# Kernel optimization log

Hardware: AMD Instinct MI355X
Metric: run time of the kernel (lower is better)

The kernel has to match this reference:

```python
import jax, jax.numpy as jnp
import numpy as np

ALPHA = 0.2        # LeakyReLU negative slope
MASK_VAL = -9e15   # matches torch zero_vec constant
B, N, F, H, D = 32, 1024, 64, 3, 16  # batch, nodes, in_features, heads, head_dim


def setup_inputs() -> dict:
    key = jax.random.key(0)
    k1, k2, k3 = jax.random.split(key, 3)
    h = jax.random.normal(k1, (B, N, F), dtype=jnp.float32)
    adj = jnp.ones((N, N), dtype=jnp.float32)  # fully-connected graph ('full')
    W = jax.random.normal(k2, (H, F, D), dtype=jnp.float32) * 0.15  # ~xavier gain 1.414
    a = jax.random.normal(k3, (H, 2 * D, 1), dtype=jnp.float32) * 0.25
    return {"h": h, "adj": adj, "W": W, "a": a}


def reference(h, adj, W, a):
    # Multi-head GAT, vectorized over heads (original loops over heads).
    d = W.shape[-1]
    Wh = jnp.einsum('bnf,hfd->bhnd', h, W)              # (B,H,N,D)
    a1 = a[:, :d, 0]                                    # (H,D) -> applies to source node i
    a2 = a[:, d:, 0]                                    # (H,D) -> applies to target node j
    s1 = jnp.einsum('bhnd,hd->bhn', Wh, a1)             # (B,H,N)
    s2 = jnp.einsum('bhnd,hd->bhn', Wh, a2)             # (B,H,N)
    # e[b,h,i,j] = LeakyReLU(a1.Wh_i + a2.Wh_j) -- equivalent to the repeat/concat trick
    e = jax.nn.leaky_relu(s1[..., :, None] + s2[..., None, :], ALPHA)  # (B,H,N,N)
    e = jnp.where(adj > 0, e, MASK_VAL)
    attn = jax.nn.softmax(e, axis=-1)                   # softmax over neighbors j
    out = jnp.einsum('bhij,bhjd->bhid', attn, Wh)       # (B,H,N,D)
    # concat heads along feature dim: (B,N,H*D)
    Bn, Nn = h.shape[0], h.shape[1]
    return out.transpose(0, 2, 1, 3).reshape(Bn, Nn, -1)
```

## Files before the change

### kernel.cpp

```cpp
#include <hip/hip_runtime.h>
#include <math.h>

constexpr int Bc = 32, Nn = 1024, Fc = 64, Hc = 3, Dc = 16;
constexpr float ALPHAc = 0.2f;
constexpr float L2E    = 1.44269504088896340736f;

__device__ __forceinline__ unsigned enc_f32(float x) {
    unsigned b = __builtin_bit_cast(unsigned, x);
    return (b & 0x80000000u) ? ~b : (b | 0x80000000u);
}
__device__ __forceinline__ float dec_f32(unsigned e) {
    unsigned b = (e & 0x80000000u) ? (e ^ 0x80000000u) : ~e;
    return __builtin_bit_cast(float, b);
}

template <int CTRL, int RMASK, bool BC>
__device__ __forceinline__ float dpp_acc(float x) {
    int s = __builtin_amdgcn_update_dpp(0, __builtin_bit_cast(int, x),
                                        CTRL, RMASK, 0xF, BC);
    return x + __builtin_bit_cast(float, s);
}
__device__ __forceinline__ float wave_incl_scan(float x) {
    x = dpp_acc<0x111, 0xF, true >(x);
    x = dpp_acc<0x112, 0xF, true >(x);
    x = dpp_acc<0x114, 0xF, true >(x);
    x = dpp_acc<0x118, 0xF, true >(x);
    x = dpp_acc<0x142, 0xa, false>(x);
    x = dpp_acc<0x143, 0xc, false>(x);
    return x;
}

__global__ __launch_bounds__(1024, 8) void gat_one(
    const float* __restrict__ hbuf, const float* __restrict__ W,
    const float* __restrict__ a, const float* __restrict__ adj,
    unsigned* __restrict__ rowful, float* __restrict__ out)
{
    __shared__ __align__(16) float    PS[1025 * 11];
    __shared__ __align__(16) unsigned skA[Nn], skB[Nn];
    __shared__ __align__(16) float    s2o[Nn];
    __shared__ __align__(16) float    whs[Nn][5];
    __shared__ float    wtot[16][10];
    __shared__ unsigned wmiss[16];

    int gid = blockIdx.x;
    int bh  = gid >> 2, q = gid & 3;
    int hh  = bh % Hc,  b = bh / Hc;
    int t   = threadIdx.x;
    int wv  = t >> 6, lane = t & 63;

    int row0 = gid * 3;
    unsigned miss = 0;
#pragma unroll
    for (int rr = 0; rr < 3; ++rr) {
        int row = row0 + rr;
        if (row < Nn) {
            float av = adj[(size_t)row * Nn + t];
            miss |= (av > 0.f) ? 0u : (1u << rr);
        }
    }
#pragma unroll
    for (int off = 1; off < 64; off <<= 1)
        miss |= (unsigned)__shfl_xor((int)miss, off, 64);
    if (lane == 0) wmiss[wv] = miss;
    __syncthreads();
    if (t < 3) {
        int row = row0 + t;
        if (row < Nn) {
            unsigned m = 0;
#pragma unroll
            for (int w2 = 0; w2 < 16; ++w2) m |= wmiss[w2];
            unsigned full = ((m >> t) & 1u) ^ 1u;
            unsigned val  = 0x5AFE0000u | ((unsigned)row << 1) | full;
            __hip_atomic_store(&rowful[row], val, __ATOMIC_RELAXED,
                               __HIP_MEMORY_SCOPE_AGENT);
        }
    }

    const float4* h4 = (const float4*)(hbuf + ((size_t)b * Nn + t) * Fc);
    const float*  Wp = W + (size_t)hh * Fc * Dc;

    float acc[Dc];
#pragma unroll
    for (int d = 0; d < Dc; ++d) acc[d] = 0.f;

#pragma unroll
    for (int qq = 0; qq < Fc / 4; ++qq) {
        float4 hv = h4[qq];
#pragma unroll
        for (int c = 0; c < 4; ++c) {
            float hv1 = (c == 0) ? hv.x : (c == 1) ? hv.y : (c == 2) ? hv.z : hv.w;
            const float4* wrp = (const float4*)(Wp + (4 * qq + c) * Dc);
#pragma unroll
            for (int u = 0; u < 4; ++u) {
                float4 wq = wrp[u];
                acc[4*u+0] = fmaf(hv1, wq.x, acc[4*u+0]);
                acc[4*u+1] = fmaf(hv1, wq.y, acc[4*u+1]);
                acc[4*u+2] = fmaf(hv1, wq.z, acc[4*u+2]);
                acc[4*u+3] = fmaf(hv1, wq.w, acc[4*u+3]);
            }
        }
    }

#pragma unroll
    for (int c = 0; c < 4; ++c)
        whs[t][c] = acc[q * 4 + c];

    const float* ap = a + (size_t)hh * 2 * Dc;
    float s1v = 0.f, s2v = 0.f;
#pragma unroll
    for (int d = 0; d < Dc; ++d) {
        s1v = fmaf(acc[d], ap[d],      s1v);
        s2v = fmaf(acc[d], ap[Dc + d], s2v);
    }
    s2o[t] = s2v;

    unsigned key = (enc_f32(s2v) & ~1023u) | (unsigned)t;

#pragma unroll
    for (int k = 2; k <= 64; k <<= 1) {
#pragma unroll
        for (int s = k >> 1; s >= 1; s >>= 1) {
            unsigned other = (unsigned)__shfl_xor((int)key, s, 64);
            bool dirUp = ((t & k) == 0);
            bool lower = ((lane & s) == 0);
            unsigned mn = key < other ? key : other;
            unsigned mx = key < other ? other : key;
            key = (lower == dirUp) ? mn : mx;
        }
    }
    unsigned* bufs[2] = {skA, skB};
    int pb = 0;
#pragma unroll
    for (int k = 128; k <= 1024; k <<= 1) {
#pragma unroll
        for (int s = k >> 1; s >= 64; s >>= 1) {
            bufs[pb][t] = key;
            __syncthreads();
            unsigned other = bufs[pb][t ^ s];
            bool dirUp = ((t & k) == 0);
            bool lower = ((t & s) == 0);
            unsigned mn = key < other ? key : other;
            unsigned mx = key < other ? other : key;
            key = (lower == dirUp) ? mn : mx;
            pb ^= 1;
        }
#pragma unroll
        for (int s = 32; s >= 1; s >>= 1) {
            unsigned other = (unsigned)__shfl_xor((int)key, s, 64);
            bool dirUp = ((t & k) == 0);
            bool lower = ((lane & s) == 0);
            unsigned mn = key < other ? key : other;
            unsigned mx = key < other ? other : key;
            key = (lower == dirUp) ? mn : mx;
        }
    }
    unsigned* sorted = bufs[pb];
    sorted[t] = key;

    int   j  = key & 1023u;
    float sv = dec_f32((key & ~1023u) | 512u);
    float Bv = __builtin_amdgcn_exp2f(sv * L2E);
    float Dv = __builtin_amdgcn_exp2f(sv * (ALPHAc * L2E));
    float w0 = whs[j][0], w1 = whs[j][1], w2 = whs[j][2], w3 = whs[j][3];

    float v[10] = {Bv * w0, Bv * w1, Bv * w2, Bv * w3,
                   Dv * w0, Dv * w1, Dv * w2, Dv * w3, Bv, Dv};

#pragma unroll
    for (int c = 0; c < 10; ++c) {
        float inc = wave_incl_scan(v[c]);
        if (lane == 63) wtot[wv][c] = inc;
        v[c] = inc - v[c];
    }
    __syncthreads();

    if (t < 160) {
        int c = t >> 4, w = t & 15;
        float own = wtot[w][c];
        float x = own;
#pragma unroll
        for (int off = 1; off < 16; off <<= 1) {
            float o = __shfl_up(x, off, 16);
            if ((lane & 15) >= off) x += o;
        }
        wtot[w][c] = x - own;
        if (w == 15) PS[(size_t)1024 * 11 + c] = x;
    }
    __syncthreads();

    float* myrow = PS + (size_t)t * 11;
#pragma unroll
    for (int c = 0; c < 10; ++c)
        myrow[c] = v[c] + wtot[wv][c];
    __syncthreads();

    int i = t;
    float R  = __builtin_amdgcn_exp2f(-0.8f * L2E * s1v);
    float* op = out + ((size_t)b * Nn + i) * (Hc * Dc) + hh * Dc + q * 4;

    unsigned expv = 0x5AFE0000u | ((unsigned)i << 1) | 1u;
    unsigned fv;
    do {
        fv = __hip_atomic_load(&rowful[i], __ATOMIC_RELAXED,
                               __HIP_MEMORY_SCOPE_AGENT);
    } while ((fv | 1u) != expv);

    if (fv & 1u) {
        unsigned qk = (enc_f32(-s1v) & ~1023u) | 1023u;
        int p = 0;
#pragma unroll
        for (int step = 512; step >= 1; step >>= 1)
            if (sorted[p + step - 1] <= qk) p += step;

        const float* Pp = PS + (size_t)p * 11;
        const float* Tp = PS + (size_t)1024 * 11;
        float den = (Tp[8] - Pp[8]) + R * Pp[9];
        float inv = 1.0f / den;
        float o0 = ((Tp[0] - Pp[0]) + R * Pp[4]) * inv;
        float o1 = ((Tp[1] - Pp[1]) + R * Pp[5]) * inv;
        float o2 = ((Tp[2] - Pp[2]) + R * Pp[6]) * inv;
        float o3 = ((Tp[3] - Pp[3]) + R * Pp[7]) * inv;
        *(float4*)op = make_float4(o0, o1, o2, o3);
    } else {
        float num[4] = {0.f, 0.f, 0.f, 0.f};
        float den = 0.f;
        for (int jj = 0; jj < Nn; ++jj) {
            float aq = adj[(size_t)i * Nn + jj];
            if (aq > 0.f) {
                float sq = s2o[jj];
                float Bq = __builtin_amdgcn_exp2f(sq * L2E);
                float Dq = __builtin_amdgcn_exp2f(sq * (ALPHAc * L2E));
                float w_ = fmaxf(Bq, R * Dq);
                den += w_;
#pragma unroll
                for (int c = 0; c < 4; ++c)
                    num[c] = fmaf(w_, whs[jj][c], num[c]);
            }
        }
        float inv = 1.0f / den;
        *(float4*)op = make_float4(num[0]*inv, num[1]*inv, num[2]*inv, num[3]*inv);
    }
}

extern "C" void kernel_launch(void* const* d_in, const int* in_sizes, int n_in,
                              void* d_out, int out_size, void* d_ws, size_t ws_size,
                              hipStream_t stream)
{
    const float* hbuf = (const float*)d_in[0];
    const float* adj  = (const float*)d_in[1];
    const float* W    = (const float*)d_in[2];
    const float* a    = (const float*)d_in[3];
    float* out = (float*)d_out;

    unsigned* rowful = (unsigned*)d_ws;

    gat_one<<<dim3(Bc * Hc * 4), dim3(1024), 0, stream>>>(
        hbuf, W, a, adj, rowful, out);
}
```

Measured before the change: 41.40 us.

## Remap block indexing, prefetch h chunks, use DPP lane swaps and float4 shared Wh

Block-to-(batch, head, quarter) mapping is permuted so consecutive blocks span different batches, and only the first 256 blocks check adjacency rows, four rows each. The input feature loads are software-prefetched chunk by chunk, the smallest bitonic sort shuffles use DPP quad permutes instead of ds_bpermute, and the shared Wh slice becomes a float4 array for vector LDS access. These aim to cut shuffle latency, LDS bank traffic and load stalls. The skipped per-block barrier in non-checking blocks and the changed block order could affect how the rowful spin-wait resolves.

```diff
diff --git a/kernel.cpp b/kernel.cpp
--- a/kernel.cpp
+++ b/kernel.cpp
@@ -30,6 +30,14 @@
     return x;
 }
 
+__device__ __forceinline__ unsigned lane_xor(unsigned x, int s) {
+    if (s == 1)
+        return (unsigned)__builtin_amdgcn_update_dpp(0, (int)x, 0xB1, 0xF, 0xF, true);
+    if (s == 2)
+        return (unsigned)__builtin_amdgcn_update_dpp(0, (int)x, 0x4E, 0xF, 0xF, true);
+    return (unsigned)__shfl_xor((int)x, s, 64);
+}
+
 __global__ __launch_bounds__(1024, 8) void gat_one(
     const float* __restrict__ hbuf, const float* __restrict__ W,
     const float* __restrict__ a, const float* __restrict__ adj,
@@ -38,38 +46,38 @@
     __shared__ __align__(16) float    PS[1025 * 11];
     __shared__ __align__(16) unsigned skA[Nn], skB[Nn];
     __shared__ __align__(16) float    s2o[Nn];
-    __shared__ __align__(16) float    whs[Nn][5];
+    __shared__ __align__(16) float4   whs4[Nn];
     __shared__ float    wtot[16][10];
     __shared__ unsigned wmiss[16];
 
-    int gid = blockIdx.x;
-    int bh  = gid >> 2, q = gid & 3;
-    int hh  = bh % Hc,  b = bh / Hc;
-    int t   = threadIdx.x;
-    int wv  = t >> 6, lane = t & 63;
-
-    int row0 = gid * 3;
-    unsigned miss = 0;
-#pragma unroll
-    for (int rr = 0; rr < 3; ++rr) {
-        int row = row0 + rr;
-        if (row < Nn) {
-            float av = adj[(size_t)row * Nn + t];
+    int p  = blockIdx.x;
+    int xq = p & 7, m = p >> 3;
+    int b  = xq + 8 * (m / 12);
+    int hq = m % 12;
+    int hh = hq >> 2, q = hq & 3;
+    int bh = b * Hc + hh;
+    int t  = threadIdx.x;
+    int wv = t >> 6, lane = t & 63;
+    (void)bh;
+
+    if (p < 256) {
+        unsigned miss = 0;
+#pragma unroll
+        for (int rr = 0; rr < 4; ++rr) {
+            float av = adj[(size_t)(p * 4 + rr) * Nn + t];
             miss |= (av > 0.f) ? 0u : (1u << rr);
         }
-    }
-#pragma unroll
-    for (int off = 1; off < 64; off <<= 1)
-        miss |= (unsigned)__shfl_xor((int)miss, off, 64);
-    if (lane == 0) wmiss[wv] = miss;
-    __syncthreads();
-    if (t < 3) {
-        int row = row0 + t;
-        if (row < Nn) {
-            unsigned m = 0;
-#pragma unroll
-            for (int w2 = 0; w2 < 16; ++w2) m |= wmiss[w2];
-            unsigned full = ((m >> t) & 1u) ^ 1u;
+#pragma unroll
+        for (int off = 1; off < 64; off <<= 1)
+            miss |= (unsigned)__shfl_xor((int)miss, off, 64);
+        if (lane == 0) wmiss[wv] = miss;
+        __syncthreads();
+        if (t < 4) {
+            unsigned mm = 0;
+#pragma unroll
+            for (int w2 = 0; w2 < 16; ++w2) mm |= wmiss[w2];
+            int row = p * 4 + t;
+            unsigned full = ((mm >> t) & 1u) ^ 1u;
             unsigned val  = 0x5AFE0000u | ((unsigned)row << 1) | full;
             __hip_atomic_store(&rowful[row], val, __ATOMIC_RELAXED,
                                __HIP_MEMORY_SCOPE_AGENT);
@@ -83,27 +91,43 @@
 #pragma unroll
     for (int d = 0; d < Dc; ++d) acc[d] = 0.f;
 
-#pragma unroll
-    for (int qq = 0; qq < Fc / 4; ++qq) {
-        float4 hv = h4[qq];
-#pragma unroll
-        for (int c = 0; c < 4; ++c) {
-            float hv1 = (c == 0) ? hv.x : (c == 1) ? hv.y : (c == 2) ? hv.z : hv.w;
-            const float4* wrp = (const float4*)(Wp + (4 * qq + c) * Dc);
-#pragma unroll
-            for (int u = 0; u < 4; ++u) {
-                float4 wq = wrp[u];
-                acc[4*u+0] = fmaf(hv1, wq.x, acc[4*u+0]);
-                acc[4*u+1] = fmaf(hv1, wq.y, acc[4*u+1]);
-                acc[4*u+2] = fmaf(hv1, wq.z, acc[4*u+2]);
-                acc[4*u+3] = fmaf(hv1, wq.w, acc[4*u+3]);
+    float4 cA[4];
+#pragma unroll
+    for (int u = 0; u < 4; ++u) cA[u] = h4[u];
+
+#pragma unroll
+    for (int ch = 0; ch < 4; ++ch) {
+        float4 cB[4];
+        if (ch < 3) {
+#pragma unroll
+            for (int u = 0; u < 4; ++u) cB[u] = h4[4 * (ch + 1) + u];
+        }
+#pragma unroll
+        for (int u = 0; u < 4; ++u) {
+            float4 hv = cA[u];
+#pragma unroll
+            for (int c = 0; c < 4; ++c) {
+                float hv1 = (c == 0) ? hv.x : (c == 1) ? hv.y
+                          : (c == 2) ? hv.z : hv.w;
+                int f = ch * 16 + u * 4 + c;
+                const float4* wrp = (const float4*)(Wp + f * Dc);
+#pragma unroll
+                for (int w = 0; w < 4; ++w) {
+                    float4 wq = wrp[w];
+                    acc[4*w+0] = fmaf(hv1, wq.x, acc[4*w+0]);
+                    acc[4*w+1] = fmaf(hv1, wq.y, acc[4*w+1]);
+                    acc[4*w+2] = fmaf(hv1, wq.z, acc[4*w+2]);
+                    acc[4*w+3] = fmaf(hv1, wq.w, acc[4*w+3]);
+                }
             }
         }
-    }
-
-#pragma unroll
-    for (int c = 0; c < 4; ++c)
-        whs[t][c] = acc[q * 4 + c];
+        if (ch < 3) {
+#pragma unroll
+            for (int u = 0; u < 4; ++u) cA[u] = cB[u];
+        }
+    }
+
+    whs4[t] = make_float4(acc[q*4+0], acc[q*4+1], acc[q*4+2], acc[q*4+3]);
 
     const float* ap = a + (size_t)hh * 2 * Dc;
     float s1v = 0.f, s2v = 0.f;
@@ -120,7 +144,7 @@
     for (int k = 2; k <= 64; k <<= 1) {
 #pragma unroll
         for (int s = k >> 1; s >= 1; s >>= 1) {
-            unsigned other = (unsigned)__shfl_xor((int)key, s, 64);
+            unsigned other = lane_xor(key, s);
             bool dirUp = ((t & k) == 0);
             bool lower = ((lane & s) == 0);
             unsigned mn = key < other ? key : other;
@@ -146,7 +170,7 @@
         }
 #pragma unroll
         for (int s = 32; s >= 1; s >>= 1) {
-            unsigned other = (unsigned)__shfl_xor((int)key, s, 64);
+            unsigned other = lane_xor(key, s);
             bool dirUp = ((t & k) == 0);
             bool lower = ((lane & s) == 0);
             unsigned mn = key < other ? key : other;
@@ -161,10 +185,10 @@
     float sv = dec_f32((key & ~1023u) | 512u);
     float Bv = __builtin_amdgcn_exp2f(sv * L2E);
     float Dv = __builtin_amdgcn_exp2f(sv * (ALPHAc * L2E));
-    float w0 = whs[j][0], w1 = whs[j][1], w2 = whs[j][2], w3 = whs[j][3];
-
-    float v[10] = {Bv * w0, Bv * w1, Bv * w2, Bv * w3,
-                   Dv * w0, Dv * w1, Dv * w2, Dv * w3, Bv, Dv};
+    float4 wsl = whs4[j];
+
+    float v[10] = {Bv * wsl.x, Bv * wsl.y, Bv * wsl.z, Bv * wsl.w,
+                   Dv * wsl.x, Dv * wsl.y, Dv * wsl.z, Dv * wsl.w, Bv, Dv};
 
 #pragma unroll
     for (int c = 0; c < 10; ++c) {
@@ -207,12 +231,12 @@
 
     if (fv & 1u) {
         unsigned qk = (enc_f32(-s1v) & ~1023u) | 1023u;
-        int p = 0;
+        int pp = 0;
 #pragma unroll
         for (int step = 512; step >= 1; step >>= 1)
-            if (sorted[p + step - 1] <= qk) p += step;
-
-        const float* Pp = PS + (size_t)p * 11;
+            if (sorted[pp + step - 1] <= qk) pp += step;
+
+        const float* Pp = PS + (size_t)pp * 11;
         const float* Tp = PS + (size_t)1024 * 11;
         float den = (Tp[8] - Pp[8]) + R * Pp[9];
         float inv = 1.0f / den;
@@ -232,9 +256,11 @@
                 float Dq = __builtin_amdgcn_exp2f(sq * (ALPHAc * L2E));
                 float w_ = fmaxf(Bq, R * Dq);
                 den += w_;
-#pragma unroll
-                for (int c = 0; c < 4; ++c)
-                    num[c] = fmaf(w_, whs[jj][c], num[c]);
+                float4 ws = whs4[jj];
+                num[0] = fmaf(w_, ws.x, num[0]);
+                num[1] = fmaf(w_, ws.y, num[1]);
+                num[2] = fmaf(w_, ws.z, num[2]);
+                num[3] = fmaf(w_, ws.w, num[3]);
             }
         }
         float inv = 1.0f / den;
```

Result: faster. 36.66 us (-11.5%).
